# Optimization experiments

Measured on AMD Instinct MI355X. Metric: run time of the kernel, lower is better.

## Reference

```python
import jax, jax.numpy as jnp
import numpy as np

D = 1024        # d_model
H = 16          # query heads
HKV = 4         # kv heads (GQA)
HD = D // H     # head dim = 64
MAX_T = 1024
EPS = 1e-6
CAP = 50.0      # logit softcap


def _rope_cache(max_t, hd):
    inv = 1.0 / (10000.0 ** (np.arange(0, hd, 2, dtype=np.float32) / hd))  # (hd/2,)
    t = np.arange(max_t, dtype=np.float32)
    f = np.outer(t, inv)                                                   # (max_t, hd/2)
    return jnp.asarray(np.cos(f)), jnp.asarray(np.sin(f))


def setup_inputs() -> dict:
    key = jax.random.key(0)
    ks = jax.random.split(key, 5)
    x = jax.random.normal(ks[0], (2, 64, 256, D), jnp.float32)  # (B,T,S,D)
    wq = jax.random.normal(ks[1], (D, H * HD), jnp.float32) * 0.02
    wk = jax.random.normal(ks[2], (D, HKV * HD), jnp.float32) * 0.02
    wv = jax.random.normal(ks[3], (D, HKV * HD), jnp.float32) * 0.02
    wo = jax.random.normal(ks[4], (H * HD, D), jnp.float32) * 0.02
    q_scale = jnp.ones((HD,), jnp.float32)  # QKNorm learnable gains
    k_scale = jnp.ones((HD,), jnp.float32)
    rope_cos, rope_sin = _rope_cache(MAX_T, HD)
    return {"x": x, "wq": wq, "wk": wk, "wv": wv, "wo": wo,
            "q_scale": q_scale, "k_scale": k_scale,
            "rope_cos": rope_cos, "rope_sin": rope_sin}


def _rmsnorm(v, scale):
    return v * jax.lax.rsqrt(jnp.mean(v * v, axis=-1, keepdims=True) + EPS) * scale


def reference(x, wq, wk, wv, wo, q_scale, k_scale, rope_cos, rope_sin):
    B, T, S, Dm = x.shape
    # fold spatial positions into batch: each position attends causally over time
    xt = x.transpose(0, 2, 1, 3).reshape(B * S, T, Dm)          # (N,T,D)
    q = (xt @ wq).reshape(B * S, T, H, HD)
    k = (xt @ wk).reshape(B * S, T, HKV, HD)
    v = (xt @ wv).reshape(B * S, T, HKV, HD)
    # QK-norm (RMSNorm over head_dim) before RoPE
    q = _rmsnorm(q, q_scale)
    k = _rmsnorm(k, k_scale)
    # 1D RoPE over temporal positions (split-half convention)
    cos = rope_cos[:T][None, :, None, :]                        # (1,T,1,HD/2)
    sin = rope_sin[:T][None, :, None, :]

    def rot(u):
        u1, u2 = jnp.split(u, 2, axis=-1)
        return jnp.concatenate([u1 * cos - u2 * sin, u1 * sin + u2 * cos], axis=-1)

    q = rot(q)
    k = rot(k)
    # GQA: expand kv heads to match query heads
    rep = H // HKV
    k = jnp.repeat(k, rep, axis=2)
    v = jnp.repeat(v, rep, axis=2)
    scores = jnp.einsum('nthd,nshd->nhts', q, k) / np.float32(np.sqrt(HD))
    scores = CAP * jnp.tanh(scores / CAP)                        # logit softcap
    causal = jnp.tril(jnp.ones((T, T), bool))
    scores = jnp.where(causal, scores, jnp.float32(-1e30))
    a = jax.nn.softmax(scores, axis=-1)
    o = jnp.einsum('nhts,nshd->nthd', a, v).reshape(B * S, T, H * HD) @ wo
    return o.reshape(B, S, T, Dm).transpose(0, 2, 1, 3)          # (B,T,S,D)
```

## Files before the change

kernel.cpp:

```cpp
#include <hip/hip_runtime.h>

#define DM   1024
#define NHQ  16
#define NKVH 4
#define HDIM 64
#define TTT  64
#define SSS  256
#define NBB  2
#define MROWS 32768

using short8 = __attribute__((ext_vector_type(8))) short;
using f32x4  = __attribute__((ext_vector_type(4))) float;

__device__ __forceinline__ short f2bf(float f) {
  union { float f; unsigned u; } v; v.f = f;
  unsigned r = v.u + 0x7fffu + ((v.u >> 16) & 1u);
  return (short)(r >> 16);
}

__device__ __forceinline__ f32x4 mfma16(short8 a, short8 b, f32x4 c) {
  return __builtin_amdgcn_mfma_f32_16x16x32_bf16(a, b, c, 0, 0, 0);
}

__device__ __forceinline__ void gload_lds16(const void* g, void* l) {
  __builtin_amdgcn_global_load_lds(
      (const __attribute__((address_space(1))) void*)g,
      (__attribute__((address_space(3))) void*)l, 16, 0, 0);
}

__global__ __launch_bounds__(256) void k_xconv(const float* __restrict__ x,
                                               short* __restrict__ xb) {
  int r = blockIdx.x;
  int n = r >> 6, t = r & 63;
  int b = n >> 8, s = n & 255;
  const float4* src = (const float4*)(x + ((size_t)((b * TTT + t) * SSS + s)) * DM);
  short4* dst = (short4*)(xb + (size_t)r * DM);
  float4 v = src[threadIdx.x];
  short4 o;
  o.x = f2bf(v.x); o.y = f2bf(v.y); o.z = f2bf(v.z); o.w = f2bf(v.w);
  dst[threadIdx.x] = o;
}

__global__ __launch_bounds__(256) void k_wt(const float* __restrict__ w,
                                            short* __restrict__ wt, int cols) {
  __shared__ float tile[32][33];
  int ctiles = cols >> 5;
  int tj = blockIdx.x % ctiles;
  int td = blockIdx.x / ctiles;
  int lx = threadIdx.x & 31, ly = threadIdx.x >> 5;
  #pragma unroll
  for (int rr = 0; rr < 32; rr += 8)
    tile[rr + ly][lx] = w[(size_t)(td * 32 + rr + ly) * cols + tj * 32 + lx];
  __syncthreads();
  #pragma unroll
  for (int rr = 0; rr < 32; rr += 8)
    wt[(size_t)(tj * 32 + rr + ly) * 1024 + td * 32 + lx] = f2bf(tile[lx][rr + ly]);
}

#define GEMM256_BODY(Ab, Bb)                                                   \
  const int tid = threadIdx.x, lane = tid & 63, wid = tid >> 6;                \
  const int wr = wid >> 2, wc = wid & 3;                                       \
  const int ln15 = lane & 15, lhi = lane >> 4;                                 \
  f32x4 acc[8][4] = {};                                                        \
  auto STAGE = [&](short* dA, short* dB, int kt) {                             \
    _Pragma("unroll")                                                          \
    for (int rr = 0; rr < 4; ++rr) {                                           \
      int c = rr * 512 + tid;                                                  \
      int row = c >> 3, c8 = c & 7;                                            \
      gload_lds16(Ab + (size_t)row * 1024 + kt + c8 * 8, dA + c * 8);          \
      gload_lds16(Bb + (size_t)row * 1024 + kt + c8 * 8, dB + c * 8);          \
    }                                                                          \
  };                                                                           \
  auto COMPUTE = [&](const short* cA, const short* cB) {                       \
    _Pragma("unroll")                                                          \
    for (int kk = 0; kk < 2; ++kk) {                                           \
      const int ko = kk * 32 + lhi * 8;                                        \
      short8 a[8], b[4];                                                       \
      _Pragma("unroll")                                                        \
      for (int n = 0; n < 4; ++n)                                              \
        b[n] = *(const short8*)(cB + (wc * 64 + n * 16 + ln15) * 64 + ko);     \
      _Pragma("unroll")                                                        \
      for (int m = 0; m < 8; ++m)                                              \
        a[m] = *(const short8*)(cA + (wr * 128 + m * 16 + ln15) * 64 + ko);    \
      _Pragma("unroll")                                                        \
      for (int m = 0; m < 8; ++m)                                              \
        _Pragma("unroll")                                                      \
        for (int n = 0; n < 4; ++n) acc[m][n] = mfma16(a[m], b[n], acc[m][n]); \
    }                                                                          \
  };                                                                           \
  STAGE(sm, sm + 16384, 0);                                                    \
  __syncthreads();                                                             \
  for (int t = 0; t < 15; ++t) {                                               \
    short* cA = (t & 1) ? sm + 32768 : sm;                                     \
    short* cB = (t & 1) ? sm + 49152 : sm + 16384;                             \
    short* nA = (t & 1) ? sm : sm + 32768;                                     \
    short* nB = (t & 1) ? sm + 16384 : sm + 49152;                             \
    STAGE(nA, nB, (t + 1) * 64);                                               \
    COMPUTE(cA, cB);                                                           \
    __syncthreads();                                                           \
  }                                                                            \
  COMPUTE(sm + 32768, sm + 49152);                                             \
  __syncthreads();

__global__ __launch_bounds__(512) void k_qkv(
    const short* __restrict__ xb, const short* __restrict__ wt,
    const float* __restrict__ qscale, const float* __restrict__ kscale,
    const float* __restrict__ rcos, const float* __restrict__ rsin,
    short* __restrict__ qb, short* __restrict__ kb, short* __restrict__ vb) {
  __shared__ __align__(16) short sm[65536];
  const int bid = blockIdx.x;
  const int swz = (bid & 7) * 96 + (bid >> 3);
  const int tn = swz % 6, tm = swz / 6;
  const short* Ab = xb + (size_t)tm * 256 * 1024;
  const short* Bb = wt + (size_t)tn * 256 * 1024;
  GEMM256_BODY(Ab, Bb)

  short* ot = sm;
  if (tn < 5) {
    const float* scale = (tn < 4) ? qscale : kscale;
    float sc[4];
    #pragma unroll
    for (int n = 0; n < 4; ++n) sc[n] = scale[n * 16 + ln15];
    #pragma unroll
    for (int m = 0; m < 8; ++m) {
      #pragma unroll
      for (int j = 0; j < 4; ++j) {
        float ss = 0.f;
        #pragma unroll
        for (int n = 0; n < 4; ++n) { float v = acc[m][n][j]; ss += v * v; }
        #pragma unroll
        for (int off = 8; off; off >>= 1) ss += __shfl_xor(ss, off, 64);
        float rms = rsqrtf(ss * (1.f / 64.f) + 1e-6f);
        int rl = wr * 128 + m * 16 + lhi * 4 + j;
        int t = (tm * 256 + rl) & 63;
        #pragma unroll
        for (int n = 0; n < 2; ++n) {
          int i = n * 16 + ln15;
          float cs = rcos[t * 32 + i], sn = rsin[t * 32 + i];
          float v1 = acc[m][n][j] * rms * sc[n];
          float v2 = acc[m][n + 2][j] * rms * sc[n + 2];
          ot[rl * 256 + wc * 64 + i]      = f2bf(v1 * cs - v2 * sn);
          ot[rl * 256 + wc * 64 + i + 32] = f2bf(v1 * sn + v2 * cs);
        }
      }
    }
  } else {
    #pragma unroll
    for (int m = 0; m < 8; ++m)
      #pragma unroll
      for (int n = 0; n < 4; ++n)
        #pragma unroll
        for (int j = 0; j < 4; ++j) {
          int rl = wr * 128 + m * 16 + lhi * 4 + j;
          ot[rl * 256 + wc * 64 + n * 16 + ln15] = f2bf(acc[m][n][j]);
        }
  }
  __syncthreads();
  {
    int row = tid >> 1, half = tid & 1;
    int r = tm * 256 + row;
    const uint4* src = (const uint4*)(ot + row * 256 + half * 128);
    short* dst;
    if (tn < 4)       dst = qb + (size_t)r * 1024 + tn * 256 + half * 128;
    else if (tn == 4) dst = kb + (size_t)r * 256 + half * 128;
    else              dst = vb + (size_t)r * 256 + half * 128;
    uint4* d4 = (uint4*)dst;
    #pragma unroll
    for (int i = 0; i < 16; ++i) d4[i] = src[i];
  }
}

__global__ __launch_bounds__(256) void k_attn(const short* __restrict__ qb,
                                              const short* __restrict__ kb,
                                              const short* __restrict__ vb,
                                              short* __restrict__ ob) {
  __shared__ __align__(16) short Qs[64 * 72];
  __shared__ __align__(16) short Ks[64 * 72];
  __shared__ __align__(16) short Vt[64 * 72];
  __shared__ __align__(16) short Ps[64 * 72];
  int h = blockIdx.x & 15, n = blockIdx.x >> 4;
  int kvh = h >> 2;
  int tid = threadIdx.x, lane = tid & 63, wid = tid >> 6;
  for (int c = tid; c < 512; c += 256) {
    int row = c >> 3, c8 = c & 7;
    *(uint4*)(&Qs[row * 72 + c8 * 8]) =
        *(const uint4*)(qb + (size_t)(n * 64 + row) * 1024 + h * 64 + c8 * 8);
    *(uint4*)(&Ks[row * 72 + c8 * 8]) =
        *(const uint4*)(kb + (size_t)(n * 64 + row) * 256 + kvh * 64 + c8 * 8);
    short8 vv = *(const short8*)(vb + (size_t)(n * 64 + row) * 256 + kvh * 64 + c8 * 8);
    #pragma unroll
    for (int e = 0; e < 8; ++e) Vt[(c8 * 8 + e) * 72 + row] = vv[e];
  }
  __syncthreads();
  int ln15 = lane & 15, lhi = lane >> 4;
  f32x4 accs[4] = {};
  #pragma unroll
  for (int kk = 0; kk < 2; ++kk) {
    int ko = kk * 32 + lhi * 8;
    short8 aq = *(const short8*)(&Qs[(wid * 16 + ln15) * 72 + ko]);
    #pragma unroll
    for (int nn = 0; nn < 4; ++nn) {
      short8 bk = *(const short8*)(&Ks[(nn * 16 + ln15) * 72 + ko]);
      accs[nn] = mfma16(aq, bk, accs[nn]);
    }
  }
  int rowloc = wid * 16 + lhi * 4;
  float p[4][4];
  #pragma unroll
  for (int j = 0; j < 4; ++j) {
    int row = rowloc + j;
    float m = -3e38f;
    #pragma unroll
    for (int nn = 0; nn < 4; ++nn) {
      float s = accs[nn][j] * 0.125f;
      s = 50.f * tanhf(s * 0.02f);
      int col = nn * 16 + ln15;
      s = (col <= row) ? s : -1e30f;
      p[nn][j] = s;
      m = fmaxf(m, s);
    }
    #pragma unroll
    for (int off = 8; off; off >>= 1) m = fmaxf(m, __shfl_xor(m, off, 64));
    float sum = 0.f;
    #pragma unroll
    for (int nn = 0; nn < 4; ++nn) {
      float e = __expf(p[nn][j] - m);
      p[nn][j] = e; sum += e;
    }
    #pragma unroll
    for (int off = 8; off; off >>= 1) sum += __shfl_xor(sum, off, 64);
    float inv = 1.f / sum;
    #pragma unroll
    for (int nn = 0; nn < 4; ++nn) p[nn][j] *= inv;
  }
  #pragma unroll
  for (int nn = 0; nn < 4; ++nn)
    #pragma unroll
    for (int j = 0; j < 4; ++j)
      Ps[(rowloc + j) * 72 + nn * 16 + ln15] = f2bf(p[nn][j]);
  __syncthreads();
  f32x4 acco[4] = {};
  #pragma unroll
  for (int kk = 0; kk < 2; ++kk) {
    int ko = kk * 32 + lhi * 8;
    short8 ap = *(const short8*)(&Ps[(wid * 16 + ln15) * 72 + ko]);
    #pragma unroll
    for (int nn = 0; nn < 4; ++nn) {
      short8 bv = *(const short8*)(&Vt[(nn * 16 + ln15) * 72 + ko]);
      acco[nn] = mfma16(ap, bv, acco[nn]);
    }
  }
  #pragma unroll
  for (int nn = 0; nn < 4; ++nn)
    #pragma unroll
    for (int j = 0; j < 4; ++j) {
      int t = rowloc + j;
      ob[(size_t)(n * 64 + t) * 1024 + h * 64 + nn * 16 + ln15] = f2bf(acco[nn][j]);
    }
}

__global__ __launch_bounds__(512) void k_out(const short* __restrict__ ab,
                                             const short* __restrict__ wt,
                                             float* __restrict__ out) {
  __shared__ __align__(16) short sm[65536];
  const int bid = blockIdx.x;
  const int swz = (bid & 7) * 64 + (bid >> 3);
  const int tn = swz & 3, tm = swz >> 2;
  const short* Ab = ab + (size_t)tm * 256 * 1024;
  const short* Bb = wt + (size_t)tn * 256 * 1024;
  GEMM256_BODY(Ab, Bb)

  float* of = (float*)sm;
  #pragma unroll
  for (int ch = 0; ch < 2; ++ch) {
    if (wr == ch) {
      #pragma unroll
      for (int m = 0; m < 8; ++m)
        #pragma unroll
        for (int n = 0; n < 4; ++n)
          #pragma unroll
          for (int j = 0; j < 4; ++j)
            of[(m * 16 + lhi * 4 + j) * 256 + wc * 64 + n * 16 + ln15] = acc[m][n][j];
    }
    __syncthreads();
    {
      int row = tid >> 2, q4 = tid & 3;
      int r = tm * 256 + ch * 128 + row;
      int nseq = r >> 6, t = r & 63;
      int b = nseq >> 8, s = nseq & 255;
      float* dst = out + ((size_t)((b * TTT + t) * SSS + s)) * DM + tn * 256 + q4 * 64;
      const float4* src = (const float4*)(of + row * 256 + q4 * 64);
      float4* d4 = (float4*)dst;
      #pragma unroll
      for (int i = 0; i < 16; ++i) d4[i] = src[i];
    }
    __syncthreads();
  }
}

extern "C" void kernel_launch(void* const* d_in, const int* in_sizes, int n_in,
                              void* d_out, int out_size, void* d_ws, size_t ws_size,
                              hipStream_t stream) {
  const float* x  = (const float*)d_in[0];
  const float* wq = (const float*)d_in[1];
  const float* wk = (const float*)d_in[2];
  const float* wv = (const float*)d_in[3];
  const float* wo = (const float*)d_in[4];
  const float* qs = (const float*)d_in[5];
  const float* ks = (const float*)d_in[6];
  const float* rc = (const float*)d_in[7];
  const float* rs = (const float*)d_in[8];
  float* out = (float*)d_out;
  char* ws = (char*)d_ws;

  short* xb    = (short*)(ws);
  short* wqkvT = (short*)(ws + 67108864);
  short* woT   = (short*)(ws + 70254592);
  short* qb    = (short*)(ws + 72351744);
  short* kb    = (short*)(ws + 139460608);
  short* vb    = (short*)(ws + 156237824);
  short* ob    = xb;

  k_xconv<<<MROWS, 256, 0, stream>>>(x, xb);
  k_wt<<<1024, 256, 0, stream>>>(wq, wqkvT, 1024);
  k_wt<<<256, 256, 0, stream>>>(wk, wqkvT + (size_t)1024 * 1024, 256);
  k_wt<<<256, 256, 0, stream>>>(wv, wqkvT + (size_t)1280 * 1024, 256);
  k_wt<<<1024, 256, 0, stream>>>(wo, woT, 1024);
  k_qkv<<<768, 512, 0, stream>>>(xb, wqkvT, qs, ks, rc, rs, qb, kb, vb);
  k_attn<<<512 * 16, 256, 0, stream>>>(qb, kb, vb, ob);
  k_out<<<512, 512, 0, stream>>>(ob, woT, out);
}
```

Before: 354.5 us.

## Restructure GEMM mainloop into phased pipeline with swizzled LDS and priority hints

Replaces the simple double-buffered 256x256 GEMM mainloop with a four-phase schedule. Each phase interleaves half-tile global-to-LDS loads with MFMA groups and uses explicit barriers, waitcnt and s_setprio. LDS chunks are XOR-swizzled to avoid bank conflicts, and launch bounds now request two blocks per CU. The goal is to hide load latency and LDS conflicts behind matrix compute, at the cost of many more barriers and tighter register limits.

```diff
diff --git a/kernel.cpp b/kernel.cpp
--- a/kernel.cpp
+++ b/kernel.cpp
@@ -57,52 +57,110 @@
     wt[(size_t)(tj * 32 + rr + ly) * 1024 + td * 32 + lx] = f2bf(tile[lx][rr + ly]);
 }
 
-#define GEMM256_BODY(Ab, Bb)                                                   \
+#define GEMM256_8PH(Ab, Bb)                                                    \
   const int tid = threadIdx.x, lane = tid & 63, wid = tid >> 6;                \
   const int wr = wid >> 2, wc = wid & 3;                                       \
   const int ln15 = lane & 15, lhi = lane >> 4;                                 \
+  const int rsw = ln15 & 7;                                                    \
   f32x4 acc[8][4] = {};                                                        \
-  auto STAGE = [&](short* dA, short* dB, int kt) {                             \
-    _Pragma("unroll")                                                          \
-    for (int rr = 0; rr < 4; ++rr) {                                           \
-      int c = rr * 512 + tid;                                                  \
-      int row = c >> 3, c8 = c & 7;                                            \
-      gload_lds16(Ab + (size_t)row * 1024 + kt + c8 * 8, dA + c * 8);          \
-      gload_lds16(Bb + (size_t)row * 1024 + kt + c8 * 8, dB + c * 8);          \
+  auto SHALF = [&](const short* gb, short* lb, int half, int kt) {             \
+    _Pragma("unroll")                                                          \
+    for (int i = 0; i < 2; ++i) {                                              \
+      int c = i * 512 + tid;                                                   \
+      int row = c >> 3, slot = c & 7;                                          \
+      gload_lds16(gb + (size_t)(half * 128 + row) * 1024 + kt                  \
+                     + ((slot ^ (row & 7)) << 3),                              \
+                  lb + half * 8192 + c * 8);                                   \
     }                                                                          \
   };                                                                           \
-  auto COMPUTE = [&](const short* cA, const short* cB) {                       \
-    _Pragma("unroll")                                                          \
-    for (int kk = 0; kk < 2; ++kk) {                                           \
-      const int ko = kk * 32 + lhi * 8;                                        \
-      short8 a[8], b[4];                                                       \
+                        \
+  SHALF(Ab, sm, 0, 0); SHALF(Ab, sm, 1, 0);                                    \
+  SHALF(Bb, sm + 16384, 0, 0); SHALF(Bb, sm + 16384, 1, 0);                    \
+  SHALF(Ab, sm + 32768, 0, 64); SHALF(Ab, sm + 32768, 1, 64);                  \
+  SHALF(Bb, sm + 49152, 0, 64); SHALF(Bb, sm + 49152, 1, 64);                  \
+  asm volatile("s_waitcnt vmcnt(8)" ::: "memory");                             \
+  __builtin_amdgcn_s_barrier();                                                \
+  for (int g = 0; g < 16; ++g) {                                               \
+    short* cA = sm + (g & 1) * 32768;                                          \
+    short* cB = cA + 16384;                                                    \
+    short* nA = sm + ((g + 1) & 1) * 32768;                                    \
+    const bool iA = (g > 0) && (g < 15);                                       \
+    const bool iB = (g < 14);                                                  \
+    short8 a[4], b0[4], b1[4];                                                 \
+                       \
+    _Pragma("unroll")                                                          \
+    for (int n = 0; n < 4; ++n)                                                \
+      b0[n] = *(const short8*)(cB + (wc * 64 + n * 16 + ln15) * 64             \
+                                  + ((lhi ^ rsw) << 3));                       \
+    _Pragma("unroll")                                                          \
+    for (int m = 0; m < 4; ++m)                                                \
+      a[m] = *(const short8*)(cA + (wr * 128 + m * 16 + ln15) * 64             \
+                                 + ((lhi ^ rsw) << 3));                        \
+    if (iA) SHALF(Ab, nA, 0, (g + 1) * 64);                                    \
+    __builtin_amdgcn_s_barrier();                                              \
+    asm volatile("s_waitcnt lgkmcnt(0)" ::: "memory");                         \
+    __builtin_amdgcn_s_setprio(1);                                             \
+    _Pragma("unroll")                                                          \
+    for (int m = 0; m < 4; ++m)                                                \
+      _Pragma("unroll")                                                        \
+      for (int n = 0; n < 4; ++n) acc[m][n] = mfma16(a[m], b0[n], acc[m][n]);  \
+    __builtin_amdgcn_s_setprio(0);                                             \
+    __builtin_amdgcn_s_barrier();                                              \
+                               \
+    _Pragma("unroll")                                                          \
+    for (int m = 0; m < 4; ++m)                                                \
+      a[m] = *(const short8*)(cA + (wr * 128 + 64 + m * 16 + ln15) * 64        \
+                                 + ((lhi ^ rsw) << 3));                        \
+    if (iA) SHALF(Ab, nA, 1, (g + 1) * 64);                                    \
+    __builtin_amdgcn_s_barrier();                                              \
+    asm volatile("s_waitcnt lgkmcnt(0)" ::: "memory");                         \
+    __builtin_amdgcn_s_setprio(1);                                             \
+    _Pragma("unroll")                                                          \
+    for (int m = 0; m < 4; ++m)                                                \
       _Pragma("unroll")                                                        \
       for (int n = 0; n < 4; ++n)                                              \
-        b[n] = *(const short8*)(cB + (wc * 64 + n * 16 + ln15) * 64 + ko);     \
+        acc[4 + m][n] = mfma16(a[m], b0[n], acc[4 + m][n]);                    \
+    __builtin_amdgcn_s_setprio(0);                                             \
+    __builtin_amdgcn_s_barrier();                                              \
+                                        \
+    _Pragma("unroll")                                                          \
+    for (int n = 0; n < 4; ++n)                                                \
+      b1[n] = *(const short8*)(cB + (wc * 64 + n * 16 + ln15) * 64             \
+                                  + (((4 + lhi) ^ rsw) << 3));                 \
+    _Pragma("unroll")                                                          \
+    for (int m = 0; m < 4; ++m)                                                \
+      a[m] = *(const short8*)(cA + (wr * 128 + m * 16 + ln15) * 64             \
+                                 + (((4 + lhi) ^ rsw) << 3));                  \
+    __builtin_amdgcn_s_barrier();                                              \
+    asm volatile("s_waitcnt lgkmcnt(0)" ::: "memory");                         \
+    __builtin_amdgcn_s_setprio(1);                                             \
+    _Pragma("unroll")                                                          \
+    for (int m = 0; m < 4; ++m)                                                \
       _Pragma("unroll")                                                        \
-      for (int m = 0; m < 8; ++m)                                              \
-        a[m] = *(const short8*)(cA + (wr * 128 + m * 16 + ln15) * 64 + ko);    \
+      for (int n = 0; n < 4; ++n) acc[m][n] = mfma16(a[m], b1[n], acc[m][n]);  \
+    __builtin_amdgcn_s_setprio(0);                                             \
+    __builtin_amdgcn_s_barrier();                                              \
+                  \
+    _Pragma("unroll")                                                          \
+    for (int m = 0; m < 4; ++m)                                                \
+      a[m] = *(const short8*)(cA + (wr * 128 + 64 + m * 16 + ln15) * 64        \
+                                 + (((4 + lhi) ^ rsw) << 3));                  \
+    if (iB) { SHALF(Bb, cB, 0, (g + 2) * 64); SHALF(Bb, cB, 1, (g + 2) * 64); }\
+    __builtin_amdgcn_s_barrier();                                              \
+    asm volatile("s_waitcnt lgkmcnt(0)" ::: "memory");                         \
+    __builtin_amdgcn_s_setprio(1);                                             \
+    _Pragma("unroll")                                                          \
+    for (int m = 0; m < 4; ++m)                                                \
       _Pragma("unroll")                                                        \
-      for (int m = 0; m < 8; ++m)                                              \
-        _Pragma("unroll")                                                      \
-        for (int n = 0; n < 4; ++n) acc[m][n] = mfma16(a[m], b[n], acc[m][n]); \
-    }                                                                          \
-  };                                                                           \
-  STAGE(sm, sm + 16384, 0);                                                    \
-  __syncthreads();                                                             \
-  for (int t = 0; t < 15; ++t) {                                               \
-    short* cA = (t & 1) ? sm + 32768 : sm;                                     \
-    short* cB = (t & 1) ? sm + 49152 : sm + 16384;                             \
-    short* nA = (t & 1) ? sm : sm + 32768;                                     \
-    short* nB = (t & 1) ? sm + 16384 : sm + 49152;                             \
-    STAGE(nA, nB, (t + 1) * 64);                                               \
-    COMPUTE(cA, cB);                                                           \
-    __syncthreads();                                                           \
-  }                                                                            \
-  COMPUTE(sm + 32768, sm + 49152);                                             \
-  __syncthreads();
-
-__global__ __launch_bounds__(512) void k_qkv(
+      for (int n = 0; n < 4; ++n)                                              \
+        acc[4 + m][n] = mfma16(a[m], b1[n], acc[4 + m][n]);                    \
+    __builtin_amdgcn_s_setprio(0);                                             \
+    if (g < 14)       asm volatile("s_waitcnt vmcnt(4)" ::: "memory");         \
+    else if (g == 14) asm volatile("s_waitcnt vmcnt(0)" ::: "memory");         \
+    __builtin_amdgcn_s_barrier();                                              \
+  }
+
+__global__ __launch_bounds__(512, 2) void k_qkv(
     const short* __restrict__ xb, const short* __restrict__ wt,
     const float* __restrict__ qscale, const float* __restrict__ kscale,
     const float* __restrict__ rcos, const float* __restrict__ rsin,
@@ -113,7 +171,7 @@
   const int tn = swz % 6, tm = swz / 6;
   const short* Ab = xb + (size_t)tm * 256 * 1024;
   const short* Bb = wt + (size_t)tn * 256 * 1024;
-  GEMM256_BODY(Ab, Bb)
+  GEMM256_8PH(Ab, Bb)
 
   short* ot = sm;
   if (tn < 5) {
@@ -259,16 +317,16 @@
     }
 }
 
-__global__ __launch_bounds__(512) void k_out(const short* __restrict__ ab,
-                                             const short* __restrict__ wt,
-                                             float* __restrict__ out) {
+__global__ __launch_bounds__(512, 2) void k_out(const short* __restrict__ ab,
+                                                const short* __restrict__ wt,
+                                                float* __restrict__ out) {
   __shared__ __align__(16) short sm[65536];
   const int bid = blockIdx.x;
   const int swz = (bid & 7) * 64 + (bid >> 3);
   const int tn = swz & 3, tm = swz >> 2;
   const short* Ab = ab + (size_t)tm * 256 * 1024;
   const short* Bb = wt + (size_t)tn * 256 * 1024;
-  GEMM256_BODY(Ab, Bb)
+  GEMM256_8PH(Ab, Bb)
 
   float* of = (float*)sm;
   #pragma unroll
```

New measurement: 341.9 us. 3.6% less time.
